# Performance work log

Measured on AMD Instinct MI355X. Metric: run time of the kernel, lower is better.

## Reference

```python
import jax, jax.numpy as jnp
import numpy as np

CUTOFF = 10.0
CUTOFF_SR = 4.0
KEHALF = 7.199822675975274
OFFSET2 = 1.0
N_ATOMS = 100000
N_EDGES = 3200000


def switch_fn(d):
    # smooth poly5 switch: 1 at d=0, 0 at d>=cutoff_short_range
    x = d / CUTOFF_SR
    s = 1.0 - x * x * x * (10.0 - 15.0 * x + 6.0 * x * x)
    return jnp.where(x < 1.0, s, 0.0)


def setup_inputs() -> dict:
    key = jax.random.key(0)
    k1, k2, k3, k4, k5, k6 = jax.random.split(key, 6)
    atomic_charges = jax.random.normal(k1, (N_ATOMS,), dtype=jnp.float32)
    atomic_dipoles = jax.random.normal(k2, (N_ATOMS, 3), dtype=jnp.float32)
    atomic_quadrupoles = jax.random.normal(k3, (N_ATOMS, 3, 3), dtype=jnp.float32)
    vectors_uv = 3.0 * jax.random.normal(k4, (N_EDGES, 3), dtype=jnp.float32)
    distances_uv = jnp.linalg.norm(vectors_uv, axis=-1)  # consistent, >0, some > cutoff
    idx_u = jax.random.randint(k5, (N_EDGES,), 0, N_ATOMS, dtype=jnp.int32)
    idx_v = jax.random.randint(k6, (N_EDGES,), 0, N_ATOMS, dtype=jnp.int32)
    return {
        'atomic_charges': atomic_charges,
        'atomic_dipoles': atomic_dipoles,
        'atomic_quadrupoles': atomic_quadrupoles,
        'vectors_uv': vectors_uv,
        'distances_uv': distances_uv,
        'idx_u': idx_u,
        'idx_v': idx_v,
    }


def reference(atomic_charges, atomic_dipoles, atomic_quadrupoles,
              vectors_uv, distances_uv, idx_u, idx_v):
    d = distances_uv                                  # [E]
    d_damped = jnp.sqrt(d * d + OFFSET2)
    sw = switch_fn(d)
    chi = sw / d_damped + (1.0 - sw) / d
    cutoff2 = CUTOFF * CUTOFF
    chi_shift = 2.0 / CUTOFF - d / cutoff2

    q_u = atomic_charges[idx_u]                       # [E]
    q_v = atomic_charges[idx_v]
    Eelec = q_u * q_v * (chi - chi_shift)

    chi2 = chi * chi
    chi3 = chi2 * chi
    cutoff3 = cutoff2 * CUTOFF
    cutoff4 = cutoff3 * CUTOFF
    chi2_shift = 3.0 / cutoff2 - 2.0 * d / cutoff3
    chi3_shift = 4.0 / cutoff3 - 3.0 * d / cutoff4

    # dipole contributions
    nvec = vectors_uv / d[:, None]                    # [E,3] normalized
    dip_u = atomic_dipoles[idx_u]
    dip_v = atomic_dipoles[idx_v]
    dot_uv = jnp.sum(nvec * dip_v, axis=1)
    dot_vu = jnp.sum(nvec * dip_u, axis=1)
    Eelec_cd = 2.0 * q_u * dot_uv * (chi2 - chi2_shift)
    Eelec_dd = (jnp.sum(dip_u * dip_v, axis=1) - 3.0 * dot_uv * dot_vu) * (chi3 - chi3_shift)
    Eelec = Eelec + Eelec_cd + Eelec_dd

    # quadrupole contributions
    outer = vectors_uv[:, :, None] * vectors_uv[:, None, :]      # [E,3,3]
    trace_mean = jnp.trace(outer, axis1=-2, axis2=-1) / 3.0      # [E]
    traceless = outer - trace_mean[:, None, None] * jnp.eye(3, dtype=outer.dtype)
    traceless = traceless / (d * d)[:, None, None]
    quad_v = atomic_quadrupoles[idx_v]                           # [E,3,3]
    sum_uv = jnp.sum(traceless * quad_v, axis=(1, 2))
    Eelec = Eelec + q_u * sum_uv * (chi3 - chi3_shift)

    Eelec = KEHALF * Eelec
    return jnp.where(d <= CUTOFF, Eelec, jnp.zeros_like(Eelec))
```

## Files before the change

kernel.cpp:

```cpp
#include <hip/hip_runtime.h>
#include <hip/hip_fp16.h>


#define CUTOFF      10.0f
#define KEHALF      7.199822675975274f

typedef float    f32x4 __attribute__((ext_vector_type(4)));
typedef int      i32x4 __attribute__((ext_vector_type(4)));
typedef unsigned u32x4 __attribute__((ext_vector_type(4)));

__device__ __forceinline__ unsigned pack_h2(float a, float b) {
    return __builtin_bit_cast(unsigned, __floats2half2_rn(a, b));
}
__device__ __forceinline__ float2 unpack_h2(unsigned u) {
    return __half22float2(__builtin_bit_cast(__half2, u));
}

__global__ __launch_bounds__(256) void pack_atoms_kernel(
    const float* __restrict__ q,
    const float* __restrict__ dip,
    const float* __restrict__ quad,
    f32x4* __restrict__ table,
    int N)
{
    int i = blockIdx.x * blockDim.x + threadIdx.x;
    if (i >= N) return;
    const float* dp = dip + 3 * (size_t)i;
    const float* qp = quad + 9 * (size_t)i;

    f32x4 w0 = {q[i], dp[0], dp[1], dp[2]};

    float q00 = qp[0], q01 = qp[1], q02 = qp[2];
    float q10 = qp[3], q11 = qp[4], q12 = qp[5];
    float q20 = qp[6], q21 = qp[7], q22 = qp[8];
    float trQ3 = (q00 + q11 + q22) * (1.0f / 3.0f);

    u32x4 w1 = {pack_h2(q00 - trQ3, q11 - trQ3),
                pack_h2(q22 - trQ3, q01 + q10),
                pack_h2(q02 + q20, q12 + q21),
                0u};

    table[2 * (size_t)i + 0] = w0;
    table[2 * (size_t)i + 1] = __builtin_bit_cast(f32x4, w1);
}

__device__ __forceinline__ float edge_energy(
    float vx, float vy, float vz,
    f32x4 au, f32x4 av, u32x4 bv)
{
    float d2 = vx * vx + vy * vy + vz * vz;
    float d = sqrtf(d2);
    float inv_d = 1.0f / d;
    float inv_d2 = inv_d * inv_d;

    float x = d * 0.25f;
    float x2 = x * x;
    float x3 = x2 * x;
    float sw = 1.0f - x3 * (10.0f - 15.0f * x + 6.0f * x2);
    sw = (x < 1.0f) ? sw : 0.0f;
    float chi = sw * rsqrtf(d2 + 1.0f) + (1.0f - sw) * inv_d;

    float c1 = chi - (0.2f   - 0.01f   * d);
    float chi2 = chi * chi;
    float chi3 = chi2 * chi;
    float c2 = chi2 - (0.03f  - 0.002f  * d);
    float c3 = chi3 - (0.004f - 0.0003f * d);

    float qu = au.x, qv = av.x;
    float Ee = qu * qv * c1;

    float dot_uv = (vx * av.y + vy * av.z + vz * av.w) * inv_d;
    float dot_vu = (vx * au.y + vy * au.z + vz * au.w) * inv_d;
    float dd     = au.y * av.y + au.z * av.z + au.w * av.w;

    Ee += 2.0f * qu * dot_uv * c2;
    Ee += (dd - 3.0f * dot_uv * dot_vu) * c3;

    float2 h0 = unpack_h2(bv.x);
    float2 h1 = unpack_h2(bv.y);
    float2 h2 = unpack_h2(bv.z);
    float num = h0.x * vx * vx + h0.y * vy * vy + h1.x * vz * vz
              + h1.y * vx * vy + h2.x * vx * vz + h2.y * vy * vz;
    Ee += qu * (num * inv_d2) * c3;

    Ee *= KEHALF;
    return (d <= CUTOFF) ? Ee : 0.0f;
}

__global__ __launch_bounds__(256, 4) void damped_elec_4e(
    const f32x4* __restrict__ table,
    const float* __restrict__ vec,
    const int*   __restrict__ idx_u,
    const int*   __restrict__ idx_v,
    float*       __restrict__ out,
    int E)
{
    int t = blockIdx.x * blockDim.x + threadIdx.x;
    size_t base = 4 * (size_t)t;

    if (base + 3 < (size_t)E) {
        i32x4 u4 = __builtin_nontemporal_load((const i32x4*)(idx_u + base));
        i32x4 v4 = __builtin_nontemporal_load((const i32x4*)(idx_v + base));
        const f32x4* vp = (const f32x4*)(vec + 3 * base);
        f32x4 w0 = __builtin_nontemporal_load(vp + 0);
        f32x4 w1 = __builtin_nontemporal_load(vp + 1);
        f32x4 w2 = __builtin_nontemporal_load(vp + 2);

        int us[4] = {u4.x, u4.y, u4.z, u4.w};
        int vs[4] = {v4.x, v4.y, v4.z, v4.w};

        f32x4 au[4], av[4], bv[4];
#pragma unroll
        for (int e = 0; e < 4; ++e) {
            au[e] = table[2 * (size_t)us[e]];
            av[e] = table[2 * (size_t)vs[e] + 0];
            bv[e] = table[2 * (size_t)vs[e] + 1];
        }

        float r0 = edge_energy(w0.x, w0.y, w0.z, au[0], av[0], __builtin_bit_cast(u32x4, bv[0]));
        float r1 = edge_energy(w0.w, w1.x, w1.y, au[1], av[1], __builtin_bit_cast(u32x4, bv[1]));
        float r2 = edge_energy(w1.z, w1.w, w2.x, au[2], av[2], __builtin_bit_cast(u32x4, bv[2]));
        float r3 = edge_energy(w2.y, w2.z, w2.w, au[3], av[3], __builtin_bit_cast(u32x4, bv[3]));

        f32x4 res = {r0, r1, r2, r3};
        __builtin_nontemporal_store(res, (f32x4*)(out + base));
    } else {
        for (size_t i = base; i < (size_t)E; ++i) {
            int u = idx_u[i];
            int v = idx_v[i];
            float vx = vec[3 * i + 0];
            float vy = vec[3 * i + 1];
            float vz = vec[3 * i + 2];
            out[i] = edge_energy(vx, vy, vz,
                                 table[2 * (size_t)u],
                                 table[2 * (size_t)v],
                                 __builtin_bit_cast(u32x4, table[2 * (size_t)v + 1]));
        }
    }
}

__global__ __launch_bounds__(256) void damped_elec_unpacked(
    const float* __restrict__ q,
    const float* __restrict__ dip,
    const float* __restrict__ quad,
    const float* __restrict__ vec,
    const int*   __restrict__ idx_u,
    const int*   __restrict__ idx_v,
    float*       __restrict__ out,
    int E)
{
    int i = blockIdx.x * blockDim.x + threadIdx.x;
    if (i >= E) return;
    float vx = vec[3 * (size_t)i + 0];
    float vy = vec[3 * (size_t)i + 1];
    float vz = vec[3 * (size_t)i + 2];
    int u = idx_u[i];
    int v = idx_v[i];
    const float* pu = dip + 3 * (size_t)u;
    const float* pv = dip + 3 * (size_t)v;
    const float* pq = quad + 9 * (size_t)v;

    f32x4 au = {q[u], pu[0], pu[1], pu[2]};
    f32x4 av = {q[v], pv[0], pv[1], pv[2]};
    float trQ3 = (pq[0] + pq[4] + pq[8]) * (1.0f / 3.0f);
    u32x4 bv = {pack_h2(pq[0] - trQ3, pq[4] - trQ3),
                pack_h2(pq[8] - trQ3, pq[1] + pq[3]),
                pack_h2(pq[2] + pq[6], pq[5] + pq[7]),
                0u};
    out[i] = edge_energy(vx, vy, vz, au, av, bv);
}

extern "C" void kernel_launch(void* const* d_in, const int* in_sizes, int n_in,
                              void* d_out, int out_size, void* d_ws, size_t ws_size,
                              hipStream_t stream) {
    const float* q    = (const float*)d_in[0];
    const float* dip  = (const float*)d_in[1];
    const float* quad = (const float*)d_in[2];
    const float* vec  = (const float*)d_in[3];
    const int*   iu   = (const int*)d_in[5];
    const int*   iv   = (const int*)d_in[6];
    float* out = (float*)d_out;

    int N = in_sizes[0];
    int E = in_sizes[4];
    int block = 256;

    size_t need = (size_t)N * 32;
    if (ws_size >= need) {
        f32x4* table = (f32x4*)d_ws;
        int pgrid = (N + block - 1) / block;
        pack_atoms_kernel<<<pgrid, block, 0, stream>>>(q, dip, quad, table, N);
        int nthreads = (E + 3) / 4;
        int egrid = (nthreads + block - 1) / block;
        damped_elec_4e<<<egrid, block, 0, stream>>>(table, vec, iu, iv, out, E);
    } else {
        int egrid = (E + block - 1) / block;
        damped_elec_unpacked<<<egrid, block, 0, stream>>>(q, dip, quad, vec, iu, iv, out, E);
    }
}
```

Before: 64.17 us.

## Replace 4-edge-per-thread kernel with software-pipelined grid-stride loop

The edge kernel now uses a fixed grid of 2048 blocks with a grid-stride loop over edges, one edge per iteration. Each iteration prefetches the next edge's indices and vector while it gathers table rows for the current edge, so stream loads overlap the random gathers. This gives up the vectorized 16-byte loads and stores and the 4-way gather parallelism per thread, and drops the launch-bounds occupancy hint.

```diff
diff --git a/kernel.cpp b/kernel.cpp
--- a/kernel.cpp
+++ b/kernel.cpp
@@ -6,7 +6,6 @@
 #define KEHALF      7.199822675975274f
 
 typedef float    f32x4 __attribute__((ext_vector_type(4)));
-typedef int      i32x4 __attribute__((ext_vector_type(4)));
 typedef unsigned u32x4 __attribute__((ext_vector_type(4)));
 
 __device__ __forceinline__ unsigned pack_h2(float a, float b) {
@@ -87,7 +86,7 @@
     return (d <= CUTOFF) ? Ee : 0.0f;
 }
 
-__global__ __launch_bounds__(256, 4) void damped_elec_4e(
+__global__ __launch_bounds__(256) void damped_elec_pipe(
     const f32x4* __restrict__ table,
     const float* __restrict__ vec,
     const int*   __restrict__ idx_u,
@@ -95,47 +94,42 @@
     float*       __restrict__ out,
     int E)
 {
-    int t = blockIdx.x * blockDim.x + threadIdx.x;
-    size_t base = 4 * (size_t)t;
+    int tid = blockIdx.x * blockDim.x + threadIdx.x;
+    int stride = gridDim.x * blockDim.x;
 
-    if (base + 3 < (size_t)E) {
-        i32x4 u4 = __builtin_nontemporal_load((const i32x4*)(idx_u + base));
-        i32x4 v4 = __builtin_nontemporal_load((const i32x4*)(idx_v + base));
-        const f32x4* vp = (const f32x4*)(vec + 3 * base);
-        f32x4 w0 = __builtin_nontemporal_load(vp + 0);
-        f32x4 w1 = __builtin_nontemporal_load(vp + 1);
-        f32x4 w2 = __builtin_nontemporal_load(vp + 2);
+    size_t i = tid;
+    if (i >= (size_t)E) return;
 
-        int us[4] = {u4.x, u4.y, u4.z, u4.w};
-        int vs[4] = {v4.x, v4.y, v4.z, v4.w};
+    int u = __builtin_nontemporal_load(idx_u + i);
+    int v = __builtin_nontemporal_load(idx_v + i);
+    float vx = __builtin_nontemporal_load(vec + 3 * i + 0);
+    float vy = __builtin_nontemporal_load(vec + 3 * i + 1);
+    float vz = __builtin_nontemporal_load(vec + 3 * i + 2);
 
-        f32x4 au[4], av[4], bv[4];
-#pragma unroll
-        for (int e = 0; e < 4; ++e) {
-            au[e] = table[2 * (size_t)us[e]];
-            av[e] = table[2 * (size_t)vs[e] + 0];
-            bv[e] = table[2 * (size_t)vs[e] + 1];
+    for (;;) {
+        size_t inext = i + (size_t)stride;
+        bool more = inext < (size_t)E;
+
+        f32x4 au = table[2 * (size_t)u];
+        f32x4 av = table[2 * (size_t)v + 0];
+        f32x4 bq = table[2 * (size_t)v + 1];
+
+        int un = 0, vn = 0;
+        float nx = 0.f, ny = 0.f, nz = 0.f;
+        if (more) {
+            un = __builtin_nontemporal_load(idx_u + inext);
+            vn = __builtin_nontemporal_load(idx_v + inext);
+            nx = __builtin_nontemporal_load(vec + 3 * inext + 0);
+            ny = __builtin_nontemporal_load(vec + 3 * inext + 1);
+            nz = __builtin_nontemporal_load(vec + 3 * inext + 2);
         }
 
-        float r0 = edge_energy(w0.x, w0.y, w0.z, au[0], av[0], __builtin_bit_cast(u32x4, bv[0]));
-        float r1 = edge_energy(w0.w, w1.x, w1.y, au[1], av[1], __builtin_bit_cast(u32x4, bv[1]));
-        float r2 = edge_energy(w1.z, w1.w, w2.x, au[2], av[2], __builtin_bit_cast(u32x4, bv[2]));
-        float r3 = edge_energy(w2.y, w2.z, w2.w, au[3], av[3], __builtin_bit_cast(u32x4, bv[3]));
+        float r = edge_energy(vx, vy, vz, au, av, __builtin_bit_cast(u32x4, bq));
+        __builtin_nontemporal_store(r, out + i);
 
-        f32x4 res = {r0, r1, r2, r3};
-        __builtin_nontemporal_store(res, (f32x4*)(out + base));
-    } else {
-        for (size_t i = base; i < (size_t)E; ++i) {
-            int u = idx_u[i];
-            int v = idx_v[i];
-            float vx = vec[3 * i + 0];
-            float vy = vec[3 * i + 1];
-            float vz = vec[3 * i + 2];
-            out[i] = edge_energy(vx, vy, vz,
-                                 table[2 * (size_t)u],
-                                 table[2 * (size_t)v],
-                                 __builtin_bit_cast(u32x4, table[2 * (size_t)v + 1]));
-        }
+        if (!more) break;
+        i = inext;
+        u = un; v = vn; vx = nx; vy = ny; vz = nz;
     }
 }
 
@@ -190,9 +184,8 @@
         f32x4* table = (f32x4*)d_ws;
         int pgrid = (N + block - 1) / block;
         pack_atoms_kernel<<<pgrid, block, 0, stream>>>(q, dip, quad, table, N);
-        int nthreads = (E + 3) / 4;
-        int egrid = (nthreads + block - 1) / block;
-        damped_elec_4e<<<egrid, block, 0, stream>>>(table, vec, iu, iv, out, E);
+        int egrid = 2048;
+        damped_elec_pipe<<<egrid, block, 0, stream>>>(table, vec, iu, iv, out, E);
     } else {
         int egrid = (E + block - 1) / block;
         damped_elec_unpacked<<<egrid, block, 0, stream>>>(q, dip, quad, vec, iu, iv, out, E);
```

Result: faster. 56.38 us (-12.1%).
